# Kernel optimization log

Measured on AMD Instinct MI355X. Metric: run time of the kernel, lower is better.

## Reference

```python
import jax, jax.numpy as jnp
import numpy as np

B, N, S, D, H, ITERS = 32, 4096, 24, 256, 4, 3
DH = D // H
SCALE = DH ** -0.5
EPS = 1e-8
LN_EPS = 1e-5


def _ln(x, g, b):
    m = x.mean(-1, keepdims=True)
    v = ((x - m) ** 2).mean(-1, keepdims=True)
    return (x - m) * jax.lax.rsqrt(v + LN_EPS) * g + b


def setup_inputs() -> dict:
    key = jax.random.key(0)
    ks = jax.random.split(key, 20)
    xav = lambda k, fi, fo: jax.random.uniform(k, (fi, fo), jnp.float32, -1.0, 1.0) * np.sqrt(6.0 / (fi + fo))
    u = lambda k, shp, fan: jax.random.uniform(k, shp, jnp.float32, -1.0, 1.0) / np.sqrt(fan)
    return {
        "extracted_features": jax.random.normal(ks[0], (B, N, D), jnp.float32),
        "conditioning": jax.random.normal(ks[1], (B, S, D), jnp.float32),
        "pos_ln_g": jnp.ones((D,), jnp.float32),
        "pos_ln_b": jnp.zeros((D,), jnp.float32),
        "pos_w1": xav(ks[2], D, D),
        "pos_b1": jnp.zeros((D,), jnp.float32),
        "pos_w2": xav(ks[3], D, D),
        "pos_b2": jnp.zeros((D,), jnp.float32),
        "in_ln_g": jnp.ones((D,), jnp.float32),
        "in_ln_b": jnp.zeros((D,), jnp.float32),
        "slot_ln_g": jnp.ones((D,), jnp.float32),
        "slot_ln_b": jnp.zeros((D,), jnp.float32),
        "Wq": u(ks[4], (D, D), D),
        "Wk": u(ks[5], (D, D), D),
        "Wv": u(ks[6], (D, D), D),
        "gru_wi": u(ks[7], (D, 3 * D), D),  # x @ gru_wi, torch weight_ih.T
        "gru_wh": u(ks[8], (D, 3 * D), D),
        "gru_bi": u(ks[9], (3 * D,), D),
        "gru_bh": u(ks[10], (3 * D,), D),
    }


def reference(extracted_features, conditioning, pos_ln_g, pos_ln_b, pos_w1, pos_b1,
              pos_w2, pos_b2, in_ln_g, in_ln_b, slot_ln_g, slot_ln_b,
              Wq, Wk, Wv, gru_wi, gru_wh, gru_bi, gru_bh):
    b, n, _ = extracted_features.shape
    s = conditioning.shape[1]
    # positional embedding MLP: LN -> Linear -> ReLU -> Linear
    feats = _ln(extracted_features, pos_ln_g, pos_ln_b)
    feats = jax.nn.relu(feats @ pos_w1 + pos_b1) @ pos_w2 + pos_b2
    # slot attention input norm + k/v projections
    inp = _ln(feats, in_ln_g, in_ln_b)
    k = (inp @ Wk).reshape(b, n, H, DH)
    v = (inp @ Wv).reshape(b, n, H, DH)

    slots = conditioning
    attn_before = None
    for _ in range(ITERS):
        slots_prev = slots
        sn = _ln(slots, slot_ln_g, slot_ln_b)
        q = (sn @ Wq).reshape(b, s, H, DH)
        dots = jnp.einsum('bihd,bjhd->bihj', q, k) * SCALE  # [b,s,H,n]
        # softmax over flattened (slot, head) axis per input token
        attn = jax.nn.softmax(dots.reshape(b, s * H, n), axis=1).reshape(b, s, H, n)
        attn_before = attn
        attn_r = (attn + EPS)
        attn_r = attn_r / attn_r.sum(-1, keepdims=True)
        updates = jnp.einsum('bjhd,bihj->bihd', v, attn_r).reshape(b * s, D)
        # GRUCell update
        h = slots_prev.reshape(b * s, D)
        gi = updates @ gru_wi + gru_bi
        gh = h @ gru_wh + gru_bh
        ir, iz, inn = jnp.split(gi, 3, axis=-1)
        hr, hz, hn = jnp.split(gh, 3, axis=-1)
        r = jax.nn.sigmoid(ir + hr)
        z = jax.nn.sigmoid(iz + hz)
        nn_ = jnp.tanh(inn + r * hn)
        slots = ((1.0 - z) * nn_ + z * h).reshape(b, s, D)

    return slots, attn_before.mean(axis=2)
```

## Files before the change

### kernel.cpp

```cpp
#include <hip/hip_runtime.h>
#include <hip/hip_bf16.h>
#include <stdint.h>

typedef __hip_bfloat16 bf16;
typedef __attribute__((ext_vector_type(8))) short short8;
typedef __attribute__((ext_vector_type(4))) float floatx4;

#define DEV __device__ __forceinline__

DEV float bf2f(bf16 v) { return __bfloat162float(v); }
DEV bf16 f2b(float f) { return __float2bfloat16(f); }
DEV unsigned short f2bu(float f) {
  bf16 h = __float2bfloat16(f);
  union { bf16 h; unsigned short u; } c; c.h = h; return c.u;
}
DEV bool is_bf16_in(const void* probe) { return ((const unsigned short*)probe)[0] != 0; }


__global__ __launch_bounds__(256) void params_kernel(
    const void* s0, const void* s1, const void* s2, const void* s3, const void* s4,
    const void* s5, const void* s6, const void* s7, const void* s8, const void* s9,
    float* dst)
{
  int idx = blockIdx.x * 256 + threadIdx.x;
  if (idx >= 3584) return;
  bool bf = is_bf16_in(s0);
  const void* srcs[10] = {s0, s1, s2, s3, s4, s5, s6, s7, s8, s9};
  int a, off;
  if (idx < 2048)      { a = idx >> 8; off = idx & 255; }
  else if (idx < 2816) { a = 8; off = idx - 2048; }
  else                 { a = 9; off = idx - 2816; }
  float v = bf ? bf2f(((const bf16*)srcs[a])[off]) : ((const float*)srcs[a])[off];
  dst[idx] = v;
}

__global__ __launch_bounds__(256) void transpose_all_kernel(
    const void* w1, const void* w2, const void* wq, const void* wk, const void* wv,
    const void* gwi, const void* gwh,
    bf16* d1, bf16* d2, bf16* dq, bf16* dk, bf16* dv, bf16* dgi, bf16* dgh,
    const void* probe)
{
  int idx = blockIdx.x * 256 + threadIdx.x;
  if (idx >= 720896) return;
  bool bf = is_bf16_in(probe);
  const void* src; bf16* dst; int C, off;
  if (idx < 327680) {
    int wsel = idx >> 16; off = idx & 65535; C = 256;
    const void* S[5] = {w1, w2, wq, wk, wv};
    bf16* D[5] = {d1, d2, dq, dk, dv};
    src = S[wsel]; dst = D[wsel];
  } else {
    int j = idx - 327680; int wsel = j / 196608; off = j - wsel * 196608; C = 768;
    src = wsel ? gwh : gwi; dst = wsel ? dgh : dgi;
  }
  int r = off / C, c = off - r * C;
  bf16 v = bf ? ((const bf16*)src)[off] : f2b(((const float*)src)[off]);
  dst[(size_t)c * 256 + r] = v;
}

__global__ __launch_bounds__(256) void init_slots_kernel(
    const void* __restrict__ cond, float* __restrict__ sF, bf16* __restrict__ sB,
    const void* probe)
{
  int idx = blockIdx.x * 256 + threadIdx.x;
  bool bf = is_bf16_in(probe);
  float v = bf ? bf2f(((const bf16*)cond)[idx]) : ((const float*)cond)[idx];
  sF[idx] = v;
  sB[idx] = f2b(v);
}

template<bool OUT_BF16, bool RELU, bool HAS_BIAS>
DEV void gemm_body(const bf16* __restrict__ A, const bf16* __restrict__ Bt,
                   const float* __restrict__ bias, void* __restrict__ C,
                   int M, int N, int K, int bx, int by, short* As, short* Bs)
{
  const int tid = threadIdx.x;
  const int lane = tid & 63;
  const int wave = tid >> 6;
  const int wr = wave >> 1, wc = wave & 1;
  const int m16 = lane & 15, quad = lane >> 4;
  const long m0 = (long)by * 128, n0 = (long)bx * 128;

  floatx4 acc[4][4];
#pragma unroll
  for (int i = 0; i < 4; i++)
#pragma unroll
    for (int j = 0; j < 4; j++) acc[i][j] = {0.f, 0.f, 0.f, 0.f};

  const int srow = tid >> 3;
  const int scol = (tid & 7) * 8;

  for (int kb = 0; kb < K; kb += 64) {
#pragma unroll
    for (int p = 0; p < 4; p++) {
      int row = srow + p * 32;
      uint4 av = *(const uint4*)(A + (m0 + row) * (long)K + kb + scol);
      *(uint4*)(&As[row * 72 + scol]) = av;
      uint4 bv = *(const uint4*)(Bt + (n0 + row) * (long)K + kb + scol);
      *(uint4*)(&Bs[row * 72 + scol]) = bv;
    }
    __syncthreads();
#pragma unroll
    for (int ks = 0; ks < 2; ks++) {
      short8 af[4], bfr[4];
#pragma unroll
      for (int t = 0; t < 4; t++) {
        af[t]  = *(const short8*)(&As[(wr * 64 + t * 16 + m16) * 72 + ks * 32 + quad * 8]);
        bfr[t] = *(const short8*)(&Bs[(wc * 64 + t * 16 + m16) * 72 + ks * 32 + quad * 8]);
      }
#pragma unroll
      for (int mt = 0; mt < 4; mt++)
#pragma unroll
        for (int nt = 0; nt < 4; nt++)
          acc[mt][nt] = __builtin_amdgcn_mfma_f32_16x16x32_bf16(af[mt], bfr[nt], acc[mt][nt], 0, 0, 0);
    }
    __syncthreads();
  }

#pragma unroll
  for (int mt = 0; mt < 4; mt++) {
#pragma unroll
    for (int nt = 0; nt < 4; nt++) {
      long col = n0 + wc * 64 + nt * 16 + m16;
      float bb = HAS_BIAS ? bias[col] : 0.f;
#pragma unroll
      for (int r = 0; r < 4; r++) {
        long row = m0 + wr * 64 + mt * 16 + quad * 4 + r;
        float v = acc[mt][nt][r] + bb;
        if (RELU) v = fmaxf(v, 0.f);
        if (OUT_BF16) ((bf16*)C)[row * N + col] = f2b(v);
        else          ((float*)C)[row * N + col] = v;
      }
    }
  }
}

template<bool OUT_BF16, bool RELU, bool HAS_BIAS>
__global__ __launch_bounds__(256) void gemm_kernel(
    const bf16* __restrict__ A, const bf16* __restrict__ Bt,
    const float* __restrict__ bias, void* __restrict__ C,
    int M, int N, int K)
{
  __shared__ short As[128 * 72];
  __shared__ short Bs[128 * 72];
  gemm_body<OUT_BF16, RELU, HAS_BIAS>(A, Bt, bias, C, M, N, K, blockIdx.x, blockIdx.y, As, Bs);
}

__global__ __launch_bounds__(256) void gru2_kernel(
    const bf16* __restrict__ updB, const bf16* __restrict__ sB,
    const bf16* __restrict__ gwit, const bf16* __restrict__ gwht,
    const float* __restrict__ par, float* __restrict__ gi, float* __restrict__ gh)
{
  __shared__ short As[128 * 72];
  __shared__ short Bs[128 * 72];
  if (blockIdx.z == 0)
    gemm_body<false, false, true>(updB, gwit, par + 2048, gi, 768, 768, 256,
                                  blockIdx.x, blockIdx.y, As, Bs);
  else
    gemm_body<false, false, true>(sB, gwht, par + 2816, gh, 768, 768, 256,
                                  blockIdx.x, blockIdx.y, As, Bs);
}

__global__ __launch_bounds__(512) void g1ln_kernel(
    const void* __restrict__ x, const bf16* __restrict__ w1t,
    const float* __restrict__ par, bf16* __restrict__ h1, const void* probe)
{
  __shared__ short As[128 * 256];
  const int tid = threadIdx.x;
  const int lane = tid & 63;
  const int wave = tid >> 6;
  const int wr = wave >> 2, wc = wave & 3;
  const int m16 = lane & 15, quad = lane >> 4;
  const long m0 = (long)blockIdx.x * 128;
  const bool bfin = is_bf16_in(probe);

  float4 gv = *(const float4*)(par + lane * 4);
  float4 bv = *(const float4*)(par + 256 + lane * 4);
#pragma unroll
  for (int i = 0; i < 16; i++) {
    int row = wave * 16 + i;
    float v[4];
    if (bfin) {
      uint2 u = *(const uint2*)((const bf16*)x + (m0 + row) * 256 + lane * 4);
      v[0] = __uint_as_float((u.x & 0xffffu) << 16);
      v[1] = __uint_as_float(u.x & 0xffff0000u);
      v[2] = __uint_as_float((u.y & 0xffffu) << 16);
      v[3] = __uint_as_float(u.y & 0xffff0000u);
    } else {
      float4 f = *(const float4*)((const float*)x + (m0 + row) * 256 + lane * 4);
      v[0] = f.x; v[1] = f.y; v[2] = f.z; v[3] = f.w;
    }
    float s = v[0] + v[1] + v[2] + v[3];
    float sq = v[0] * v[0] + v[1] * v[1] + v[2] * v[2] + v[3] * v[3];
#pragma unroll
    for (int off = 32; off > 0; off >>= 1) { s += __shfl_xor(s, off); sq += __shfl_xor(sq, off); }
    float mn = s * (1.f / 256.f);
    float rs = rsqrtf(sq * (1.f / 256.f) - mn * mn + 1e-5f);
    union { unsigned short us[4]; uint2 u; } pk;
    pk.us[0] = f2bu((v[0] - mn) * rs * gv.x + bv.x);
    pk.us[1] = f2bu((v[1] - mn) * rs * gv.y + bv.y);
    pk.us[2] = f2bu((v[2] - mn) * rs * gv.z + bv.z);
    pk.us[3] = f2bu((v[3] - mn) * rs * gv.w + bv.w);
    *(uint2*)(&As[row * 256 + ((lane * 4) ^ ((row & 7) << 3))]) = pk.u;
  }
  __syncthreads();

  floatx4 acc[4][4];
#pragma unroll
  for (int i = 0; i < 4; i++)
#pragma unroll
    for (int j = 0; j < 4; j++) acc[i][j] = {0.f, 0.f, 0.f, 0.f};

#pragma unroll
  for (int ks = 0; ks < 8; ks++) {
    short8 af[4], bfr[4];
#pragma unroll
    for (int t = 0; t < 4; t++) {
      int row = wr * 64 + t * 16 + m16;
      af[t] = *(const short8*)(&As[row * 256 + ((ks * 32 + quad * 8) ^ ((row & 7) << 3))]);
      bfr[t] = *(const short8*)(w1t + (size_t)(wc * 64 + t * 16 + m16) * 256 + ks * 32 + quad * 8);
    }
#pragma unroll
    for (int mt = 0; mt < 4; mt++)
#pragma unroll
      for (int nt = 0; nt < 4; nt++)
        acc[mt][nt] = __builtin_amdgcn_mfma_f32_16x16x32_bf16(af[mt], bfr[nt], acc[mt][nt], 0, 0, 0);
  }

#pragma unroll
  for (int mt = 0; mt < 4; mt++)
#pragma unroll
    for (int nt = 0; nt < 4; nt++) {
      int col = wc * 64 + nt * 16 + m16;
      float bb = par[512 + col];
#pragma unroll
      for (int r = 0; r < 4; r++) {
        long row = m0 + wr * 64 + mt * 16 + quad * 4 + r;
        h1[row * 256 + col] = f2b(fmaxf(acc[mt][nt][r] + bb, 0.f));
      }
    }
}

__global__ __launch_bounds__(512) void kvln_kernel(
    const bf16* __restrict__ feats, const bf16* __restrict__ wkt, const bf16* __restrict__ wvt,
    const float* __restrict__ par, bf16* __restrict__ kbuf, bf16* __restrict__ vT)
{
  __shared__ short As[128 * 256];
  const int tid = threadIdx.x;
  const int lane = tid & 63;
  const int wave = tid >> 6;
  const int wr = wave >> 2, wc = wave & 3;
  const int m16 = lane & 15, quad = lane >> 4;
  const long m0 = (long)blockIdx.x * 128;

#pragma unroll
  for (int i = 0; i < 8; i++) {
    int idx = tid + i * 512;
    int row = idx >> 5, col = (idx & 31) * 8;
    short8 vls = *(const short8*)(feats + (m0 + row) * 256 + col);
    *(short8*)(&As[row * 256 + (col ^ ((row & 7) << 3))]) = vls;
  }
  __syncthreads();

  float4 gv = *(const float4*)(par + 1024 + lane * 4);
  float4 bv = *(const float4*)(par + 1280 + lane * 4);
#pragma unroll
  for (int i = 0; i < 16; i++) {
    int row = wave * 16 + i;
    int ci = (lane * 4) ^ ((row & 7) << 3);
    uint2 u = *(const uint2*)(&As[row * 256 + ci]);
    float v[4];
    v[0] = __uint_as_float((u.x & 0xffffu) << 16);
    v[1] = __uint_as_float(u.x & 0xffff0000u);
    v[2] = __uint_as_float((u.y & 0xffffu) << 16);
    v[3] = __uint_as_float(u.y & 0xffff0000u);
    float s = v[0] + v[1] + v[2] + v[3];
    float sq = v[0] * v[0] + v[1] * v[1] + v[2] * v[2] + v[3] * v[3];
#pragma unroll
    for (int off = 32; off > 0; off >>= 1) { s += __shfl_xor(s, off); sq += __shfl_xor(sq, off); }
    float mn = s * (1.f / 256.f);
    float rs = rsqrtf(sq * (1.f / 256.f) - mn * mn + 1e-5f);
    union { unsigned short us[4]; uint2 u; } pk;
    pk.us[0] = f2bu((v[0] - mn) * rs * gv.x + bv.x);
    pk.us[1] = f2bu((v[1] - mn) * rs * gv.y + bv.y);
    pk.us[2] = f2bu((v[2] - mn) * rs * gv.z + bv.z);
    pk.us[3] = f2bu((v[3] - mn) * rs * gv.w + bv.w);
    *(uint2*)(&As[row * 256 + ci]) = pk.u;
  }
  __syncthreads();

#pragma unroll
  for (int proj = 0; proj < 2; proj++) {
    const bf16* W = proj ? wvt : wkt;
    floatx4 acc[4][4];
#pragma unroll
    for (int i = 0; i < 4; i++)
#pragma unroll
      for (int j = 0; j < 4; j++) acc[i][j] = {0.f, 0.f, 0.f, 0.f};
#pragma unroll
    for (int ks = 0; ks < 8; ks++) {
      short8 af[4], bfr[4];
#pragma unroll
      for (int t = 0; t < 4; t++) {
        int row = wr * 64 + t * 16 + m16;
        af[t] = *(const short8*)(&As[row * 256 + ((ks * 32 + quad * 8) ^ ((row & 7) << 3))]);
        bfr[t] = *(const short8*)(W + (size_t)(wc * 64 + t * 16 + m16) * 256 + ks * 32 + quad * 8);
      }
#pragma unroll
      for (int mt = 0; mt < 4; mt++)
#pragma unroll
        for (int nt = 0; nt < 4; nt++)
          acc[mt][nt] = __builtin_amdgcn_mfma_f32_16x16x32_bf16(af[mt], bfr[nt], acc[mt][nt], 0, 0, 0);
    }
    if (proj == 0) {
#pragma unroll
      for (int mt = 0; mt < 4; mt++)
#pragma unroll
        for (int nt = 0; nt < 4; nt++) {
          int col = wc * 64 + nt * 16 + m16;
#pragma unroll
          for (int r = 0; r < 4; r++) {
            long row = m0 + wr * 64 + mt * 16 + quad * 4 + r;
            kbuf[row * 256 + col] = f2b(acc[mt][nt][r]);
          }
        }
    } else {
#pragma unroll
      for (int mt = 0; mt < 4; mt++)
#pragma unroll
        for (int nt = 0; nt < 4; nt++) {
          int d = wc * 64 + nt * 16 + m16;
          long t0 = m0 + wr * 64 + mt * 16 + quad * 4;
          union { unsigned short us[4]; uint2 u; } pk;
#pragma unroll
          for (int r = 0; r < 4; r++) pk.us[r] = f2bu(acc[mt][nt][r]);
          *(uint2*)(vT + (size_t)d * 131072 + t0) = pk.u;
        }
    }
  }
}

__global__ __launch_bounds__(256) void lnq_kernel(
    const float* __restrict__ sF, const bf16* __restrict__ wqt,
    const float* __restrict__ par, bf16* __restrict__ qp)
{
  __shared__ short As[32 * 264];
  const int tid = threadIdx.x;
  const int lane = tid & 63;
  const int wave = tid >> 6;
  const int m16 = lane & 15, quad = lane >> 4;
  const int b = blockIdx.x;

  for (int i = tid; i < 8 * 264; i += 256) As[24 * 264 + i] = 0;

  float4 gv = *(const float4*)(par + 1536 + lane * 4);
  float4 bv = *(const float4*)(par + 1792 + lane * 4);
#pragma unroll
  for (int i = 0; i < 6; i++) {
    int row = wave * 6 + i;
    float4 f = *(const float4*)(sF + ((size_t)(b * 24 + row)) * 256 + lane * 4);
    float v[4] = {f.x, f.y, f.z, f.w};
    float s = v[0] + v[1] + v[2] + v[3];
    float sq = v[0] * v[0] + v[1] * v[1] + v[2] * v[2] + v[3] * v[3];
#pragma unroll
    for (int off = 32; off > 0; off >>= 1) { s += __shfl_xor(s, off); sq += __shfl_xor(sq, off); }
    float mn = s * (1.f / 256.f);
    float rs = rsqrtf(sq * (1.f / 256.f) - mn * mn + 1e-5f);
    union { unsigned short us[4]; uint2 u; } pk;
    pk.us[0] = f2bu((v[0] - mn) * rs * gv.x + bv.x);
    pk.us[1] = f2bu((v[1] - mn) * rs * gv.y + bv.y);
    pk.us[2] = f2bu((v[2] - mn) * rs * gv.z + bv.z);
    pk.us[3] = f2bu((v[3] - mn) * rs * gv.w + bv.w);
    *(uint2*)(&As[row * 264 + lane * 4]) = pk.u;
  }
  __syncthreads();

  floatx4 acc[2][4];
#pragma unroll
  for (int i = 0; i < 2; i++)
#pragma unroll
    for (int j = 0; j < 4; j++) acc[i][j] = {0.f, 0.f, 0.f, 0.f};
#pragma unroll
  for (int ks = 0; ks < 8; ks++) {
    short8 af[2], bfr[4];
#pragma unroll
    for (int mt = 0; mt < 2; mt++)
      af[mt] = *(const short8*)(&As[(mt * 16 + m16) * 264 + ks * 32 + quad * 8]);
#pragma unroll
    for (int nt = 0; nt < 4; nt++)
      bfr[nt] = *(const short8*)(wqt + (size_t)(wave * 64 + nt * 16 + m16) * 256 + ks * 32 + quad * 8);
#pragma unroll
    for (int mt = 0; mt < 2; mt++)
#pragma unroll
      for (int nt = 0; nt < 4; nt++)
        acc[mt][nt] = __builtin_amdgcn_mfma_f32_16x16x32_bf16(af[mt], bfr[nt], acc[mt][nt], 0, 0, 0);
  }

  bf16* qpb = qp + (size_t)(b * 4 + wave) * 2048;
#pragma unroll
  for (int mt = 0; mt < 2; mt++)
#pragma unroll
    for (int nt = 0; nt < 4; nt++)
#pragma unroll
      for (int r = 0; r < 4; r++) {
        int m = mt * 16 + quad * 4 + r;
        qpb[m * 64 + nt * 16 + m16] = f2b(acc[mt][nt][r] * 0.125f);
      }
}

template<bool LAST>
__global__ __launch_bounds__(256) void attn_iter_kernel(
    const bf16* __restrict__ qp, const bf16* __restrict__ kbuf,
    const bf16* __restrict__ vT, float* __restrict__ pupd,
    void* __restrict__ out, const void* __restrict__ probe)
{
  const int js = blockIdx.x;
  const int b  = blockIdx.y;
  const int h  = threadIdx.x >> 6;
  const int lane = threadIdx.x & 63;
  const int m16 = lane & 15, quad = lane >> 4;

  __shared__ unsigned short att[4 * 24 * 136];
  __shared__ float red1[4 * 132];
  __shared__ float red2[4 * 132];

  short8 qf[2][2];
  const bf16* qpb = qp + (size_t)(b * 4 + h) * 2048;
#pragma unroll
  for (int mt = 0; mt < 2; mt++)
#pragma unroll
    for (int ks = 0; ks < 2; ks++)
      qf[mt][ks] = *(const short8*)(qpb + (mt * 16 + m16) * 64 + ks * 32 + quad * 8);

  const bool mt1_valid = (quad < 2);
  int arow1 = 16 + m16; if (arow1 > 23) arow1 = 23;

  floatx4 uacc[2][4];
#pragma unroll
  for (int i = 0; i < 2; i++)
#pragma unroll
    for (int j = 0; j < 4; j++) uacc[i][j] = {0.f, 0.f, 0.f, 0.f};
  float wsum[2][4] = {{0.f, 0.f, 0.f, 0.f}, {0.f, 0.f, 0.f, 0.f}};

  for (int hh = 0; hh < 2; hh++) {
    const int j0 = js * 256 + hh * 128;

    floatx4 dacc[2][8];
#pragma unroll
    for (int i = 0; i < 2; i++)
#pragma unroll
      for (int j = 0; j < 8; j++) dacc[i][j] = {0.f, 0.f, 0.f, 0.f};

    const bf16* kb = kbuf + ((size_t)b * 4096 + j0) * 256 + h * 64;
#pragma unroll
    for (int ks = 0; ks < 2; ks++)
#pragma unroll
      for (int nt = 0; nt < 8; nt++) {
        short8 bfr = *(const short8*)(kb + (size_t)(nt * 16 + m16) * 256 + ks * 32 + quad * 8);
        dacc[0][nt] = __builtin_amdgcn_mfma_f32_16x16x32_bf16(qf[0][ks], bfr, dacc[0][nt], 0, 0, 0);
        dacc[1][nt] = __builtin_amdgcn_mfma_f32_16x16x32_bf16(qf[1][ks], bfr, dacc[1][nt], 0, 0, 0);
      }

    float cmax[8];
#pragma unroll
    for (int nt = 0; nt < 8; nt++) {
      float m = fmaxf(fmaxf(dacc[0][nt][0], dacc[0][nt][1]), fmaxf(dacc[0][nt][2], dacc[0][nt][3]));
      if (mt1_valid)
        m = fmaxf(m, fmaxf(fmaxf(dacc[1][nt][0], dacc[1][nt][1]), fmaxf(dacc[1][nt][2], dacc[1][nt][3])));
      m = fmaxf(m, __shfl_xor(m, 16));
      m = fmaxf(m, __shfl_xor(m, 32));
      cmax[nt] = m;
    }
    if (quad == 0) {
#pragma unroll
      for (int nt = 0; nt < 8; nt++) red1[h * 132 + nt * 16 + m16] = cmax[nt];
    }
    __syncthreads();

    float csum[8];
#pragma unroll
    for (int nt = 0; nt < 8; nt++) {
      int c = nt * 16 + m16;
      float g = fmaxf(fmaxf(red1[c], red1[132 + c]), fmaxf(red1[264 + c], red1[396 + c]));
      float s = 0.f;
#pragma unroll
      for (int r = 0; r < 4; r++) {
        float e = __expf(dacc[0][nt][r] - g);
        dacc[0][nt][r] = e; s += e;
      }
#pragma unroll
      for (int r = 0; r < 4; r++) {
        float e = mt1_valid ? __expf(dacc[1][nt][r] - g) : 0.f;
        dacc[1][nt][r] = e; s += e;
      }
      s += __shfl_xor(s, 16);
      s += __shfl_xor(s, 32);
      csum[nt] = s;
    }
    if (quad == 0) {
#pragma unroll
      for (int nt = 0; nt < 8; nt++) red2[h * 132 + nt * 16 + m16] = csum[nt];
    }
    __syncthreads();

#pragma unroll
    for (int nt = 0; nt < 8; nt++) {
      int c = nt * 16 + m16;
      float inv = 1.f / (red2[c] + red2[132 + c] + red2[264 + c] + red2[396 + c]);
#pragma unroll
      for (int r = 0; r < 4; r++) {
        float a = dacc[0][nt][r] * inv + 1e-8f;
        att[h * 3264 + (quad * 4 + r) * 136 + c] = f2bu(a);
        wsum[0][r] += a;
      }
      if (mt1_valid) {
#pragma unroll
        for (int r = 0; r < 4; r++) {
          float a = dacc[1][nt][r] * inv + 1e-8f;
          att[h * 3264 + (16 + quad * 4 + r) * 136 + c] = f2bu(a);
          wsum[1][r] += a;
        }
      }
    }
    __syncthreads();

    const bf16* vb0 = vT + (size_t)b * 4096 + j0;
#pragma unroll
    for (int ks = 0; ks < 4; ks++) {
      short8 a0 = *(const short8*)(&att[h * 3264 + m16 * 136 + ks * 32 + quad * 8]);
      short8 a1 = *(const short8*)(&att[h * 3264 + arow1 * 136 + ks * 32 + quad * 8]);
#pragma unroll
      for (int nt = 0; nt < 4; nt++) {
        short8 bfr = *(const short8*)(vb0 + (size_t)(h * 64 + nt * 16 + m16) * 131072 + ks * 32 + quad * 8);
        uacc[0][nt] = __builtin_amdgcn_mfma_f32_16x16x32_bf16(a0, bfr, uacc[0][nt], 0, 0, 0);
        uacc[1][nt] = __builtin_amdgcn_mfma_f32_16x16x32_bf16(a1, bfr, uacc[1][nt], 0, 0, 0);
      }
    }

    if (LAST) {
      const bool bfo = is_bf16_in(probe);
      int c = threadIdx.x & 127;
      int half = threadIdx.x >> 7;
#pragma unroll
      for (int i0 = 0; i0 < 12; i0++) {
        int i = half * 12 + i0;
        float s = bf2f(__ushort_as_bfloat16(att[i * 136 + c]))
                + bf2f(__ushort_as_bfloat16(att[3264 + i * 136 + c]))
                + bf2f(__ushort_as_bfloat16(att[6528 + i * 136 + c]))
                + bf2f(__ushort_as_bfloat16(att[9792 + i * 136 + c]));
        size_t oidx = ((size_t)(b * 24 + i)) * 4096 + j0 + c;
        if (bfo) ((bf16*)out)[196608 + oidx] = f2b(0.25f * s);
        else     ((float*)out)[196608 + oidx] = 0.25f * s;
      }
    }
    __syncthreads();
  }

  float* dst = pupd + ((size_t)((b * 4 + h) * 16 + js)) * 1920;
#pragma unroll
  for (int mt = 0; mt < 2; mt++)
#pragma unroll
    for (int r = 0; r < 4; r++) {
      float w = wsum[mt][r];
      w += __shfl_xor(w, 1); w += __shfl_xor(w, 2);
      w += __shfl_xor(w, 4); w += __shfl_xor(w, 8);
      wsum[mt][r] = w;
    }
  if (m16 == 0) {
#pragma unroll
    for (int mt = 0; mt < 2; mt++)
#pragma unroll
      for (int r = 0; r < 4; r++) {
        int row = mt * 16 + quad * 4 + r;
        if (row < 24) dst[row * 80 + 64] = wsum[mt][r];
      }
  }
#pragma unroll
  for (int mt = 0; mt < 2; mt++)
#pragma unroll
    for (int nt = 0; nt < 4; nt++)
#pragma unroll
      for (int r = 0; r < 4; r++) {
        int row = mt * 16 + quad * 4 + r;
        if (row < 24) dst[row * 80 + nt * 16 + m16] = uacc[mt][nt][r];
      }
}

__global__ __launch_bounds__(256) void upd_final_kernel(
    const float* __restrict__ pupd, bf16* __restrict__ updB)
{
  int bh = blockIdx.x; int b = bh >> 2, h = bh & 3;
  int idx = blockIdx.y * 256 + threadIdx.x;
  int i = idx >> 6, d = idx & 63;
  const float* base = pupd + (size_t)bh * 16 * 1920 + i * 80;
  float v = 0.f, w = 0.f;
#pragma unroll
  for (int p = 0; p < 16; p++) {
    v += base[p * 1920 + d];
    w += base[p * 1920 + 64];
  }
  updB[((size_t)(b * 24 + i)) * 256 + h * 64 + d] = f2b(v / w);
}

template<bool LAST>
__global__ __launch_bounds__(256) void gru_gate_kernel(
    const float* __restrict__ gi, const float* __restrict__ gh,
    float* __restrict__ sF, bf16* __restrict__ sB,
    void* __restrict__ out, const void* __restrict__ probe)
{
  int row = blockIdx.x, d = threadIdx.x;
  size_t o = (size_t)row * 768;
  float ir = gi[o + d], iz = gi[o + 256 + d], inn = gi[o + 512 + d];
  float hr = gh[o + d], hz = gh[o + 256 + d], hn = gh[o + 512 + d];
  float hv = sF[(size_t)row * 256 + d];
  float r = 1.f / (1.f + __expf(-(ir + hr)));
  float z = 1.f / (1.f + __expf(-(iz + hz)));
  float nn = tanhf(inn + r * hn);
  float sv = (1.f - z) * nn + z * hv;
  sF[(size_t)row * 256 + d] = sv;
  sB[(size_t)row * 256 + d] = f2b(sv);
  if (LAST) {
    if (is_bf16_in(probe)) ((bf16*)out)[(size_t)row * 256 + d] = f2b(sv);
    else                   ((float*)out)[(size_t)row * 256 + d] = sv;
  }
}

static constexpr size_t SZ_BIG   = (size_t)32 * 4096 * 256 * 2;
static constexpr size_t OFF_BUF1 = 0;
static constexpr size_t OFF_BUF2 = OFF_BUF1 + SZ_BIG;
static constexpr size_t OFF_K    = OFF_BUF2 + SZ_BIG;
static constexpr size_t OFF_V    = OFF_K + SZ_BIG;
static constexpr size_t OFF_Q    = OFF_V + SZ_BIG;
static constexpr size_t OFF_QP   = OFF_Q + (size_t)768 * 256 * 4;
static constexpr size_t OFF_SNB  = OFF_QP + (size_t)32 * 4 * 32 * 64 * 2;
static constexpr size_t OFF_SF   = OFF_SNB + (size_t)768 * 256 * 2;
static constexpr size_t OFF_SB   = OFF_SF + (size_t)768 * 256 * 4;
static constexpr size_t OFF_UPD  = OFF_SB + (size_t)768 * 256 * 2;
static constexpr size_t OFF_GI   = OFF_UPD + (size_t)768 * 256 * 2;
static constexpr size_t OFF_GH   = OFF_GI + (size_t)768 * 768 * 4;
static constexpr size_t OFF_PUPD = OFF_GH + (size_t)768 * 768 * 4;
static constexpr size_t OFF_W1T  = OFF_PUPD + (size_t)128 * 32 * 1920 * 4;
static constexpr size_t OFF_W2T  = OFF_W1T + (size_t)256 * 256 * 2;
static constexpr size_t OFF_WQT  = OFF_W2T + (size_t)256 * 256 * 2;
static constexpr size_t OFF_WKT  = OFF_WQT + (size_t)256 * 256 * 2;
static constexpr size_t OFF_WVT  = OFF_WKT + (size_t)256 * 256 * 2;
static constexpr size_t OFF_GWIT = OFF_WVT + (size_t)256 * 256 * 2;
static constexpr size_t OFF_GWHT = OFF_GWIT + (size_t)256 * 768 * 2;
static constexpr size_t OFF_PAR  = OFF_GWHT + (size_t)256 * 768 * 2;
static constexpr size_t OFF_FLAG = OFF_PAR + (size_t)3584 * 4;
static constexpr size_t WS_NEED  = OFF_FLAG + 256;

extern "C" void kernel_launch(void* const* d_in, const int* in_sizes, int n_in,
                              void* d_out, int out_size, void* d_ws, size_t ws_size,
                              hipStream_t stream) {
  (void)in_sizes; (void)n_in; (void)out_size;
  if (ws_size < WS_NEED) return;

  const void* x         = d_in[0];
  const void* cond      = d_in[1];
  const void* pos_ln_g  = d_in[2];
  const void* pos_ln_b  = d_in[3];
  const void* pos_w1    = d_in[4];
  const void* pos_b1    = d_in[5];
  const void* pos_w2    = d_in[6];
  const void* pos_b2    = d_in[7];
  const void* in_ln_g   = d_in[8];
  const void* in_ln_b   = d_in[9];
  const void* slot_ln_g = d_in[10];
  const void* slot_ln_b = d_in[11];
  const void* Wq        = d_in[12];
  const void* Wk        = d_in[13];
  const void* Wv        = d_in[14];
  const void* gru_wi    = d_in[15];
  const void* gru_wh    = d_in[16];
  const void* gru_bi    = d_in[17];
  const void* gru_bh    = d_in[18];

  char* ws = (char*)d_ws;
  bf16*  buf1  = (bf16*)(ws + OFF_BUF1);
  bf16*  buf2  = (bf16*)(ws + OFF_BUF2);
  bf16*  kbuf  = (bf16*)(ws + OFF_K);
  bf16*  vT    = (bf16*)(ws + OFF_V);
  bf16*  qp    = (bf16*)(ws + OFF_QP);
  float* sF    = (float*)(ws + OFF_SF);
  bf16*  sB    = (bf16*)(ws + OFF_SB);
  bf16*  updB  = (bf16*)(ws + OFF_UPD);
  float* gi    = (float*)(ws + OFF_GI);
  float* gh    = (float*)(ws + OFF_GH);
  float* pupd  = (float*)(ws + OFF_PUPD);
  bf16*  w1t   = (bf16*)(ws + OFF_W1T);
  bf16*  w2t   = (bf16*)(ws + OFF_W2T);
  bf16*  wqt   = (bf16*)(ws + OFF_WQT);
  bf16*  wkt   = (bf16*)(ws + OFF_WKT);
  bf16*  wvt   = (bf16*)(ws + OFF_WVT);
  bf16*  gwit  = (bf16*)(ws + OFF_GWIT);
  bf16*  gwht  = (bf16*)(ws + OFF_GWHT);
  float* par   = (float*)(ws + OFF_PAR);

  const void* probe = pos_ln_g;

  params_kernel<<<14, 256, 0, stream>>>(pos_ln_g, pos_ln_b, pos_b1, pos_b2,
                                        in_ln_g, in_ln_b, slot_ln_g, slot_ln_b,
                                        gru_bi, gru_bh, par);
  transpose_all_kernel<<<2816, 256, 0, stream>>>(pos_w1, pos_w2, Wq, Wk, Wv, gru_wi, gru_wh,
                                                 w1t, w2t, wqt, wkt, wvt, gwit, gwht, probe);
  init_slots_kernel<<<768, 256, 0, stream>>>(cond, sF, sB, probe);

  g1ln_kernel<<<1024, 512, 0, stream>>>(x, w1t, par, buf1, probe);
  gemm_kernel<true, false, true><<<dim3(2, 1024), 256, 0, stream>>>(
      buf1, w2t, par + 768, buf2, 131072, 256, 256);
  kvln_kernel<<<1024, 512, 0, stream>>>(buf2, wkt, wvt, par, kbuf, vT);

  for (int it = 0; it < 3; it++) {
    lnq_kernel<<<32, 256, 0, stream>>>(sF, wqt, par, qp);
    if (it == 2)
      attn_iter_kernel<true><<<dim3(16, 32), 256, 0, stream>>>(qp, kbuf, vT, pupd, d_out, probe);
    else
      attn_iter_kernel<false><<<dim3(16, 32), 256, 0, stream>>>(qp, kbuf, vT, pupd, d_out, probe);
    upd_final_kernel<<<dim3(128, 6), 256, 0, stream>>>(pupd, updB);
    gru2_kernel<<<dim3(6, 6, 2), 256, 0, stream>>>(updB, sB, gwit, gwht, par, gi, gh);
    if (it == 2)
      gru_gate_kernel<true><<<768, 256, 0, stream>>>(gi, gh, sF, sB, d_out, probe);
    else
      gru_gate_kernel<false><<<768, 256, 0, stream>>>(gi, gh, sF, sB, d_out, probe);
  }
}
```

Measured before the change: 651.1 us.

## Fuse LN, MLP, LN and K/V projections into one kernel

Replaces three kernels (LN+W1, generic W2 GEMM, LN+K/V projections) with a single kernel that processes 64-row tiles and keeps all intermediates in shared memory. This removes the global round trips of the two 131072x256 bf16 intermediates and two launches. The V transpose now goes through shared memory so the global vT writes are coalesced. In exchange each block does four sequential GEMMs with weights read from global memory per wave, uses smaller 64-row tiles and adds more barriers.

```diff
diff --git a/kernel.cpp b/kernel.cpp
--- a/kernel.cpp
+++ b/kernel.cpp
@@ -135,17 +135,6 @@
   }
 }
 
-template<bool OUT_BF16, bool RELU, bool HAS_BIAS>
-__global__ __launch_bounds__(256) void gemm_kernel(
-    const bf16* __restrict__ A, const bf16* __restrict__ Bt,
-    const float* __restrict__ bias, void* __restrict__ C,
-    int M, int N, int K)
-{
-  __shared__ short As[128 * 72];
-  __shared__ short Bs[128 * 72];
-  gemm_body<OUT_BF16, RELU, HAS_BIAS>(A, Bt, bias, C, M, N, K, blockIdx.x, blockIdx.y, As, Bs);
-}
-
 __global__ __launch_bounds__(256) void gru2_kernel(
     const bf16* __restrict__ updB, const bf16* __restrict__ sB,
     const bf16* __restrict__ gwit, const bf16* __restrict__ gwht,
@@ -161,181 +150,191 @@
                                   blockIdx.x, blockIdx.y, As, Bs);
 }
 
-__global__ __launch_bounds__(512) void g1ln_kernel(
-    const void* __restrict__ x, const bf16* __restrict__ w1t,
-    const float* __restrict__ par, bf16* __restrict__ h1, const void* probe)
-{
-  __shared__ short As[128 * 256];
+
+DEV void mm64(const short* As, const bf16* __restrict__ W,
+              floatx4 acc[4][4], int wave, int m16, int quad)
+{
+#pragma unroll
+  for (int ks = 0; ks < 8; ks++) {
+    short8 af[4], bfr[4];
+#pragma unroll
+    for (int t = 0; t < 4; t++) {
+      int row = t * 16 + m16;
+      af[t] = *(const short8*)(&As[row * 256 + ((ks * 32 + quad * 8) ^ ((row & 7) << 3))]);
+      bfr[t] = *(const short8*)(W + (size_t)(wave * 64 + t * 16 + m16) * 256 + ks * 32 + quad * 8);
+    }
+#pragma unroll
+    for (int mt = 0; mt < 4; mt++)
+#pragma unroll
+      for (int nt = 0; nt < 4; nt++)
+        acc[mt][nt] = __builtin_amdgcn_mfma_f32_16x16x32_bf16(af[mt], bfr[nt], acc[mt][nt], 0, 0, 0);
+  }
+}
+
+__global__ __launch_bounds__(256, 3) void phasea_kernel(
+    const void* __restrict__ x,
+    const bf16* __restrict__ w1t, const bf16* __restrict__ w2t,
+    const bf16* __restrict__ wkt, const bf16* __restrict__ wvt,
+    const float* __restrict__ par,
+    bf16* __restrict__ kbuf, bf16* __restrict__ vT, const void* probe)
+{
+  __shared__ short As[64 * 256];
   const int tid = threadIdx.x;
   const int lane = tid & 63;
   const int wave = tid >> 6;
-  const int wr = wave >> 2, wc = wave & 3;
   const int m16 = lane & 15, quad = lane >> 4;
-  const long m0 = (long)blockIdx.x * 128;
+  const long m0 = (long)blockIdx.x * 64;
   const bool bfin = is_bf16_in(probe);
 
-  float4 gv = *(const float4*)(par + lane * 4);
-  float4 bv = *(const float4*)(par + 256 + lane * 4);
-#pragma unroll
-  for (int i = 0; i < 16; i++) {
-    int row = wave * 16 + i;
-    float v[4];
-    if (bfin) {
-      uint2 u = *(const uint2*)((const bf16*)x + (m0 + row) * 256 + lane * 4);
+  {
+    float4 gv = *(const float4*)(par + lane * 4);
+    float4 bv = *(const float4*)(par + 256 + lane * 4);
+#pragma unroll
+    for (int i = 0; i < 16; i++) {
+      int row = wave * 16 + i;
+      float v[4];
+      if (bfin) {
+        uint2 u = *(const uint2*)((const bf16*)x + (m0 + row) * 256 + lane * 4);
+        v[0] = __uint_as_float((u.x & 0xffffu) << 16);
+        v[1] = __uint_as_float(u.x & 0xffff0000u);
+        v[2] = __uint_as_float((u.y & 0xffffu) << 16);
+        v[3] = __uint_as_float(u.y & 0xffff0000u);
+      } else {
+        float4 f = *(const float4*)((const float*)x + (m0 + row) * 256 + lane * 4);
+        v[0] = f.x; v[1] = f.y; v[2] = f.z; v[3] = f.w;
+      }
+      float s = v[0] + v[1] + v[2] + v[3];
+      float sq = v[0] * v[0] + v[1] * v[1] + v[2] * v[2] + v[3] * v[3];
+#pragma unroll
+      for (int off = 32; off > 0; off >>= 1) { s += __shfl_xor(s, off); sq += __shfl_xor(sq, off); }
+      float mn = s * (1.f / 256.f);
+      float rs = rsqrtf(sq * (1.f / 256.f) - mn * mn + 1e-5f);
+      union { unsigned short us[4]; uint2 u; } pk;
+      pk.us[0] = f2bu((v[0] - mn) * rs * gv.x + bv.x);
+      pk.us[1] = f2bu((v[1] - mn) * rs * gv.y + bv.y);
+      pk.us[2] = f2bu((v[2] - mn) * rs * gv.z + bv.z);
+      pk.us[3] = f2bu((v[3] - mn) * rs * gv.w + bv.w);
+      *(uint2*)(&As[row * 256 + ((lane * 4) ^ ((row & 7) << 3))]) = pk.u;
+    }
+  }
+  __syncthreads();
+
+  floatx4 acc[4][4];
+
+#pragma unroll
+  for (int i = 0; i < 4; i++)
+#pragma unroll
+    for (int j = 0; j < 4; j++) acc[i][j] = {0.f, 0.f, 0.f, 0.f};
+  mm64(As, w1t, acc, wave, m16, quad);
+  __syncthreads();
+#pragma unroll
+  for (int mt = 0; mt < 4; mt++)
+#pragma unroll
+    for (int nt = 0; nt < 4; nt++) {
+      int col = wave * 64 + nt * 16 + m16;
+      float bb = par[512 + col];
+#pragma unroll
+      for (int r = 0; r < 4; r++) {
+        int row = mt * 16 + quad * 4 + r;
+        As[row * 256 + (col ^ ((row & 7) << 3))] = (short)f2bu(fmaxf(acc[mt][nt][r] + bb, 0.f));
+      }
+    }
+  __syncthreads();
+
+#pragma unroll
+  for (int i = 0; i < 4; i++)
+#pragma unroll
+    for (int j = 0; j < 4; j++) acc[i][j] = {0.f, 0.f, 0.f, 0.f};
+  mm64(As, w2t, acc, wave, m16, quad);
+  __syncthreads();
+#pragma unroll
+  for (int mt = 0; mt < 4; mt++)
+#pragma unroll
+    for (int nt = 0; nt < 4; nt++) {
+      int col = wave * 64 + nt * 16 + m16;
+      float bb = par[768 + col];
+#pragma unroll
+      for (int r = 0; r < 4; r++) {
+        int row = mt * 16 + quad * 4 + r;
+        As[row * 256 + (col ^ ((row & 7) << 3))] = (short)f2bu(acc[mt][nt][r] + bb);
+      }
+    }
+  __syncthreads();
+
+  {
+    float4 gv = *(const float4*)(par + 1024 + lane * 4);
+    float4 bv = *(const float4*)(par + 1280 + lane * 4);
+#pragma unroll
+    for (int i = 0; i < 16; i++) {
+      int row = wave * 16 + i;
+      int ci = (lane * 4) ^ ((row & 7) << 3);
+      uint2 u = *(const uint2*)(&As[row * 256 + ci]);
+      float v[4];
       v[0] = __uint_as_float((u.x & 0xffffu) << 16);
       v[1] = __uint_as_float(u.x & 0xffff0000u);
       v[2] = __uint_as_float((u.y & 0xffffu) << 16);
       v[3] = __uint_as_float(u.y & 0xffff0000u);
-    } else {
-      float4 f = *(const float4*)((const float*)x + (m0 + row) * 256 + lane * 4);
-      v[0] = f.x; v[1] = f.y; v[2] = f.z; v[3] = f.w;
-    }
-    float s = v[0] + v[1] + v[2] + v[3];
-    float sq = v[0] * v[0] + v[1] * v[1] + v[2] * v[2] + v[3] * v[3];
-#pragma unroll
-    for (int off = 32; off > 0; off >>= 1) { s += __shfl_xor(s, off); sq += __shfl_xor(sq, off); }
-    float mn = s * (1.f / 256.f);
-    float rs = rsqrtf(sq * (1.f / 256.f) - mn * mn + 1e-5f);
-    union { unsigned short us[4]; uint2 u; } pk;
-    pk.us[0] = f2bu((v[0] - mn) * rs * gv.x + bv.x);
-    pk.us[1] = f2bu((v[1] - mn) * rs * gv.y + bv.y);
-    pk.us[2] = f2bu((v[2] - mn) * rs * gv.z + bv.z);
-    pk.us[3] = f2bu((v[3] - mn) * rs * gv.w + bv.w);
-    *(uint2*)(&As[row * 256 + ((lane * 4) ^ ((row & 7) << 3))]) = pk.u;
-  }
-  __syncthreads();
-
-  floatx4 acc[4][4];
+      float s = v[0] + v[1] + v[2] + v[3];
+      float sq = v[0] * v[0] + v[1] * v[1] + v[2] * v[2] + v[3] * v[3];
+#pragma unroll
+      for (int off = 32; off > 0; off >>= 1) { s += __shfl_xor(s, off); sq += __shfl_xor(sq, off); }
+      float mn = s * (1.f / 256.f);
+      float rs = rsqrtf(sq * (1.f / 256.f) - mn * mn + 1e-5f);
+      union { unsigned short us[4]; uint2 u; } pk;
+      pk.us[0] = f2bu((v[0] - mn) * rs * gv.x + bv.x);
+      pk.us[1] = f2bu((v[1] - mn) * rs * gv.y + bv.y);
+      pk.us[2] = f2bu((v[2] - mn) * rs * gv.z + bv.z);
+      pk.us[3] = f2bu((v[3] - mn) * rs * gv.w + bv.w);
+      *(uint2*)(&As[row * 256 + ci]) = pk.u;
+    }
+  }
+  __syncthreads();
+
 #pragma unroll
   for (int i = 0; i < 4; i++)
 #pragma unroll
     for (int j = 0; j < 4; j++) acc[i][j] = {0.f, 0.f, 0.f, 0.f};
-
-#pragma unroll
-  for (int ks = 0; ks < 8; ks++) {
-    short8 af[4], bfr[4];
-#pragma unroll
-    for (int t = 0; t < 4; t++) {
-      int row = wr * 64 + t * 16 + m16;
-      af[t] = *(const short8*)(&As[row * 256 + ((ks * 32 + quad * 8) ^ ((row & 7) << 3))]);
-      bfr[t] = *(const short8*)(w1t + (size_t)(wc * 64 + t * 16 + m16) * 256 + ks * 32 + quad * 8);
-    }
-#pragma unroll
-    for (int mt = 0; mt < 4; mt++)
-#pragma unroll
-      for (int nt = 0; nt < 4; nt++)
-        acc[mt][nt] = __builtin_amdgcn_mfma_f32_16x16x32_bf16(af[mt], bfr[nt], acc[mt][nt], 0, 0, 0);
-  }
-
+  mm64(As, wkt, acc, wave, m16, quad);
 #pragma unroll
   for (int mt = 0; mt < 4; mt++)
 #pragma unroll
     for (int nt = 0; nt < 4; nt++) {
-      int col = wc * 64 + nt * 16 + m16;
-      float bb = par[512 + col];
-#pragma unroll
-      for (int r = 0; r < 4; r++) {
-        long row = m0 + wr * 64 + mt * 16 + quad * 4 + r;
-        h1[row * 256 + col] = f2b(fmaxf(acc[mt][nt][r] + bb, 0.f));
-      }
-    }
-}
-
-__global__ __launch_bounds__(512) void kvln_kernel(
-    const bf16* __restrict__ feats, const bf16* __restrict__ wkt, const bf16* __restrict__ wvt,
-    const float* __restrict__ par, bf16* __restrict__ kbuf, bf16* __restrict__ vT)
-{
-  __shared__ short As[128 * 256];
-  const int tid = threadIdx.x;
-  const int lane = tid & 63;
-  const int wave = tid >> 6;
-  const int wr = wave >> 2, wc = wave & 3;
-  const int m16 = lane & 15, quad = lane >> 4;
-  const long m0 = (long)blockIdx.x * 128;
-
-#pragma unroll
-  for (int i = 0; i < 8; i++) {
-    int idx = tid + i * 512;
-    int row = idx >> 5, col = (idx & 31) * 8;
-    short8 vls = *(const short8*)(feats + (m0 + row) * 256 + col);
-    *(short8*)(&As[row * 256 + (col ^ ((row & 7) << 3))]) = vls;
-  }
-  __syncthreads();
-
-  float4 gv = *(const float4*)(par + 1024 + lane * 4);
-  float4 bv = *(const float4*)(par + 1280 + lane * 4);
-#pragma unroll
-  for (int i = 0; i < 16; i++) {
-    int row = wave * 16 + i;
-    int ci = (lane * 4) ^ ((row & 7) << 3);
-    uint2 u = *(const uint2*)(&As[row * 256 + ci]);
-    float v[4];
-    v[0] = __uint_as_float((u.x & 0xffffu) << 16);
-    v[1] = __uint_as_float(u.x & 0xffff0000u);
-    v[2] = __uint_as_float((u.y & 0xffffu) << 16);
-    v[3] = __uint_as_float(u.y & 0xffff0000u);
-    float s = v[0] + v[1] + v[2] + v[3];
-    float sq = v[0] * v[0] + v[1] * v[1] + v[2] * v[2] + v[3] * v[3];
-#pragma unroll
-    for (int off = 32; off > 0; off >>= 1) { s += __shfl_xor(s, off); sq += __shfl_xor(sq, off); }
-    float mn = s * (1.f / 256.f);
-    float rs = rsqrtf(sq * (1.f / 256.f) - mn * mn + 1e-5f);
-    union { unsigned short us[4]; uint2 u; } pk;
-    pk.us[0] = f2bu((v[0] - mn) * rs * gv.x + bv.x);
-    pk.us[1] = f2bu((v[1] - mn) * rs * gv.y + bv.y);
-    pk.us[2] = f2bu((v[2] - mn) * rs * gv.z + bv.z);
-    pk.us[3] = f2bu((v[3] - mn) * rs * gv.w + bv.w);
-    *(uint2*)(&As[row * 256 + ci]) = pk.u;
-  }
-  __syncthreads();
-
-#pragma unroll
-  for (int proj = 0; proj < 2; proj++) {
-    const bf16* W = proj ? wvt : wkt;
-    floatx4 acc[4][4];
-#pragma unroll
-    for (int i = 0; i < 4; i++)
-#pragma unroll
-      for (int j = 0; j < 4; j++) acc[i][j] = {0.f, 0.f, 0.f, 0.f};
-#pragma unroll
-    for (int ks = 0; ks < 8; ks++) {
-      short8 af[4], bfr[4];
-#pragma unroll
-      for (int t = 0; t < 4; t++) {
-        int row = wr * 64 + t * 16 + m16;
-        af[t] = *(const short8*)(&As[row * 256 + ((ks * 32 + quad * 8) ^ ((row & 7) << 3))]);
-        bfr[t] = *(const short8*)(W + (size_t)(wc * 64 + t * 16 + m16) * 256 + ks * 32 + quad * 8);
-      }
-#pragma unroll
-      for (int mt = 0; mt < 4; mt++)
-#pragma unroll
-        for (int nt = 0; nt < 4; nt++)
-          acc[mt][nt] = __builtin_amdgcn_mfma_f32_16x16x32_bf16(af[mt], bfr[nt], acc[mt][nt], 0, 0, 0);
-    }
-    if (proj == 0) {
-#pragma unroll
-      for (int mt = 0; mt < 4; mt++)
-#pragma unroll
-        for (int nt = 0; nt < 4; nt++) {
-          int col = wc * 64 + nt * 16 + m16;
-#pragma unroll
-          for (int r = 0; r < 4; r++) {
-            long row = m0 + wr * 64 + mt * 16 + quad * 4 + r;
-            kbuf[row * 256 + col] = f2b(acc[mt][nt][r]);
-          }
-        }
-    } else {
-#pragma unroll
-      for (int mt = 0; mt < 4; mt++)
-#pragma unroll
-        for (int nt = 0; nt < 4; nt++) {
-          int d = wc * 64 + nt * 16 + m16;
-          long t0 = m0 + wr * 64 + mt * 16 + quad * 4;
-          union { unsigned short us[4]; uint2 u; } pk;
-#pragma unroll
-          for (int r = 0; r < 4; r++) pk.us[r] = f2bu(acc[mt][nt][r]);
-          *(uint2*)(vT + (size_t)d * 131072 + t0) = pk.u;
-        }
+      int col = wave * 64 + nt * 16 + m16;
+#pragma unroll
+      for (int r = 0; r < 4; r++) {
+        long row = m0 + mt * 16 + quad * 4 + r;
+        kbuf[row * 256 + col] = f2b(acc[mt][nt][r]);
+      }
+    }
+
+#pragma unroll
+  for (int i = 0; i < 4; i++)
+#pragma unroll
+    for (int j = 0; j < 4; j++) acc[i][j] = {0.f, 0.f, 0.f, 0.f};
+  mm64(As, wvt, acc, wave, m16, quad);
+  __syncthreads();
+#pragma unroll
+  for (int mt = 0; mt < 4; mt++)
+#pragma unroll
+    for (int nt = 0; nt < 4; nt++) {
+      int d = wave * 64 + nt * 16 + m16;
+      int t = mt * 16 + quad * 4;
+      union { unsigned short us[4]; uint2 u; } pk;
+#pragma unroll
+      for (int r = 0; r < 4; r++) pk.us[r] = f2bu(acc[mt][nt][r]);
+      *(uint2*)(&As[d * 64 + (t ^ ((d & 15) << 2))]) = pk.u;
+    }
+  __syncthreads();
+
+  {
+    int sub = lane >> 4;
+    int mcol = lane & 15;
+#pragma unroll
+    for (int j = 0; j < 16; j++) {
+      int d = wave * 64 + j * 4 + sub;
+      int t = mcol * 4;
+      uint2 u = *(const uint2*)(&As[d * 64 + (t ^ ((d & 15) << 2))]);
+      *(uint2*)(vT + (size_t)d * 131072 + m0 + t) = u;
     }
   }
 }
@@ -677,8 +676,6 @@
   const void* gru_bh    = d_in[18];
 
   char* ws = (char*)d_ws;
-  bf16*  buf1  = (bf16*)(ws + OFF_BUF1);
-  bf16*  buf2  = (bf16*)(ws + OFF_BUF2);
   bf16*  kbuf  = (bf16*)(ws + OFF_K);
   bf16*  vT    = (bf16*)(ws + OFF_V);
   bf16*  qp    = (bf16*)(ws + OFF_QP);
@@ -706,10 +703,7 @@
                                                  w1t, w2t, wqt, wkt, wvt, gwit, gwht, probe);
   init_slots_kernel<<<768, 256, 0, stream>>>(cond, sF, sB, probe);
 
-  g1ln_kernel<<<1024, 512, 0, stream>>>(x, w1t, par, buf1, probe);
-  gemm_kernel<true, false, true><<<dim3(2, 1024), 256, 0, stream>>>(
-      buf1, w2t, par + 768, buf2, 131072, 256, 256);
-  kvln_kernel<<<1024, 512, 0, stream>>>(buf2, wkt, wvt, par, kbuf, vT);
+  phasea_kernel<<<2048, 256, 0, stream>>>(x, w1t, w2t, wkt, wvt, par, kbuf, vT, probe);
 
   for (int it = 0; it < 3; it++) {
     lnq_kernel<<<32, 256, 0, stream>>>(sF, wqt, par, qp);
```

New measurement: 674.1 us. +3.5%, slower.
